# Performance work log

Measured on AMD Instinct MI355X. Metric: run time of the kernel, lower is better.

Reference implementation:

```python
import jax, jax.numpy as jnp
import numpy as np

E, H, NH, FFN, OUT = 4096, 512, 4, 1024, 1
HD = H // NH
LN_EPS = 1e-5


def setup_inputs() -> dict:
    key = jax.random.key(0)
    ks = jax.random.split(key, 20)
    s = 1.0 / np.sqrt(H)
    inp = {
        'x': jax.random.normal(ks[0], (E, H), jnp.float32),
        'edge_index': jax.random.randint(ks[1], (2, E), 0, E, jnp.int64),
        # DMPNN message linear
        'W_msg': jax.random.normal(ks[2], (H, H), jnp.float32) * s,
        'b_msg': jnp.zeros((H,), jnp.float32),
        # GRUCell weights (torch layout: [3H, H], gates r,z,n)
        'W_ih': jax.random.normal(ks[3], (3 * H, H), jnp.float32) * s,
        'b_ih': jnp.zeros((3 * H,), jnp.float32),
        'W_hh': jax.random.normal(ks[4], (3 * H, H), jnp.float32) * s,
        'b_hh': jnp.zeros((3 * H,), jnp.float32),
        # MultiheadAttention combined in-proj [3H, H] and out-proj [H, H]
        'W_in_proj': jax.random.normal(ks[5], (3 * H, H), jnp.float32) * s,
        'b_in_proj': jnp.zeros((3 * H,), jnp.float32),
        'W_out_proj': jax.random.normal(ks[6], (H, H), jnp.float32) * s,
        'b_out_proj': jnp.zeros((H,), jnp.float32),
        # LayerNorm
        'ln_g': jnp.ones((H,), jnp.float32),
        'ln_b': jnp.zeros((H,), jnp.float32),
        # GlobalAttention output linear
        'W_lin': jax.random.normal(ks[7], (H, H), jnp.float32) * s,
        'b_lin': jnp.zeros((H,), jnp.float32),
        # FFN: Linear(H->FFN), ReLU, Linear(FFN->OUT)
        'W_f1': jax.random.normal(ks[8], (FFN, H), jnp.float32) * s,
        'b_f1': jnp.zeros((FFN,), jnp.float32),
        'W_f2': jax.random.normal(ks[9], (OUT, FFN), jnp.float32) * (1.0 / np.sqrt(FFN)),
        'b_f2': jnp.zeros((OUT,), jnp.float32),
    }
    return inp


def reference(x, edge_index, W_msg, b_msg, W_ih, b_ih, W_hh, b_hh,
              W_in_proj, b_in_proj, W_out_proj, b_out_proj, ln_g, ln_b,
              W_lin, b_lin, W_f1, b_f1, W_f2, b_f2):
    # ---- DMPNNLayer: message + scatter-add aggregation + GRUCell update ----
    msg = jax.nn.relu(x @ W_msg.T + b_msg)                       # [E, H]
    agg = jnp.zeros_like(x).at[edge_index[1]].add(msg)           # scatter-add to dst edges
    gi = agg @ W_ih.T + b_ih                                     # [E, 3H]
    gh = x @ W_hh.T + b_hh                                       # [E, 3H]
    ir, iz, inn = jnp.split(gi, 3, axis=-1)
    hr, hz, hn = jnp.split(gh, 3, axis=-1)
    r = jax.nn.sigmoid(ir + hr)
    z = jax.nn.sigmoid(iz + hz)
    n = jnp.tanh(inn + r * hn)
    h = (1.0 - z) * n + z * x                                    # [E, H] updated edges
    # ---- GlobalAttention: MHA(h,h,h) + residual LN + relu(linear) ----
    qkv = h @ W_in_proj.T + b_in_proj                            # [E, 3H]
    q, k, v = jnp.split(qkv, 3, axis=-1)
    split_heads = lambda t: t.reshape(E, NH, HD).transpose(1, 0, 2)  # [NH, E, HD]
    q, k, v = split_heads(q), split_heads(k), split_heads(v)
    scale = np.float32(1.0 / np.sqrt(HD))
    attn = jax.nn.softmax(jnp.einsum('hqd,hkd->hqk', q, k) * scale, axis=-1)
    o = jnp.einsum('hqk,hkd->hqd', attn, v).transpose(1, 0, 2).reshape(E, H)
    o = o @ W_out_proj.T + b_out_proj
    y = o + h
    mu = jnp.mean(y, axis=-1, keepdims=True)
    var = jnp.mean((y - mu) ** 2, axis=-1, keepdims=True)
    yn = (y - mu) / jnp.sqrt(var + LN_EPS) * ln_g + ln_b
    g = jax.nn.relu(yn @ W_lin.T + b_lin)                        # [E, H]
    # ---- FFN ----
    f = jax.nn.relu(g @ W_f1.T + b_f1)                           # [E, FFN]
    return f @ W_f2.T + b_f2                                     # [E, OUT]
```

## Files before the change

### kernel.cpp

```cpp
#include <hip/hip_runtime.h>

typedef unsigned short ushort_t;
typedef __attribute__((ext_vector_type(8))) short short8;
typedef __attribute__((ext_vector_type(4))) float float4v;

#define E_N   4096
#define H_N   512
#define NH_N  4
#define HD_N  128
#define FFN_N 1024
#define H3_N  1536

__device__ __forceinline__ float bf2f(ushort_t u) {
  union { unsigned u; float f; } v; v.u = ((unsigned)u) << 16; return v.f;
}
__device__ __forceinline__ ushort_t f2bf(float f) {
  union { float f; unsigned u; } v; v.f = f;
  unsigned r = v.u + 0x7fffu + ((v.u >> 16) & 1u);
  return (ushort_t)(r >> 16);
}
__device__ __forceinline__ float fexp2(float x) {
  return __builtin_amdgcn_exp2f(x);
}
__device__ __forceinline__ uint4 cvt8(const float* p) {
  float4 a = *(const float4*)p;
  float4 b = *(const float4*)(p + 4);
  union { ushort_t u[8]; uint4 v; } pk;
  pk.u[0] = f2bf(a.x); pk.u[1] = f2bf(a.y); pk.u[2] = f2bf(a.z); pk.u[3] = f2bf(a.w);
  pk.u[4] = f2bf(b.x); pk.u[5] = f2bf(b.y); pk.u[6] = f2bf(b.z); pk.u[7] = f2bf(b.w);
  return pk.v;
}

__device__ __forceinline__ void gload16(const void* g, void* l) {
  __builtin_amdgcn_global_load_lds(
      (const __attribute__((address_space(1))) unsigned*)g,
      (__attribute__((address_space(3))) unsigned*)l, 16, 0, 0);
}

__global__ __launch_bounds__(256) void prep_kernel(
    const float* __restrict__ x,
    const float* __restrict__ wmsg, const float* __restrict__ wih,
    const float* __restrict__ whh,  const float* __restrict__ win,
    const float* __restrict__ wout, const float* __restrict__ wlin,
    const float* __restrict__ wf1,  ushort_t* __restrict__ dst,
    float4* __restrict__ agg)
{
  int b = blockIdx.x;
  if (b < 2048) {
    agg[(size_t)b * 256 + threadIdx.x] = make_float4(0.f, 0.f, 0.f, 0.f);
    return;
  }
  size_t o = ((size_t)(b - 2048) * 256 + threadIdx.x) * 8;
  const float* s;
  if      (o < 2097152) s = x    + o;
  else if (o < 2359296) s = wmsg + (o - 2097152);
  else if (o < 3145728) s = wih  + (o - 2359296);
  else if (o < 3932160) s = whh  + (o - 3145728);
  else if (o < 4718592) s = win  + (o - 3932160);
  else if (o < 4980736) s = wout + (o - 4718592);
  else if (o < 5242880) s = wlin + (o - 4980736);
  else                  s = wf1  + (o - 5242880);
  *(uint4*)(dst + o) = cvt8(s);
}

__global__ __launch_bounds__(256) void cvt_agg_kernel(
    const float* __restrict__ agg, ushort_t* __restrict__ aggb) {
  size_t o = ((size_t)blockIdx.x * 256 + threadIdx.x) * 8;
  *(uint4*)(aggb + o) = cvt8(agg + o);
}

__global__ __launch_bounds__(256) void f2red_kernel(
    const float* __restrict__ pf, const float* __restrict__ b2,
    float* __restrict__ out) {
  int i = blockIdx.x * 256 + threadIdx.x;
  float s = b2[0];
#pragma unroll
  for (int k = 0; k < 32; k++) s += pf[(size_t)i * 32 + k];
  out[i] = s;
}

__global__ __launch_bounds__(256) void amerge_kernel(
    const float* __restrict__ po0, const float* __restrict__ po1,
    const float* __restrict__ mlg, ushort_t* __restrict__ ob) {
  int t = blockIdx.x * 256 + threadIdx.x;
  int row = t >> 6;
  int c8  = (t & 63) * 8;
  int head = c8 >> 7;
  const float* p0 = mlg + ((size_t)(0 * 4 + head) * E_N + row) * 2;
  const float* p1 = mlg + ((size_t)(1 * 4 + head) * E_N + row) * 2;
  float m0 = p0[0], l0 = p0[1], m1 = p1[0], l1 = p1[1];
  float m  = fmaxf(m0, m1);
  float e0 = fexp2(m0 - m), e1 = fexp2(m1 - m);
  float inv = 1.f / (l0 * e0 + l1 * e1);
  float s0 = e0 * inv, s1 = e1 * inv;
  size_t off = (size_t)row * H_N + c8;
  float4 a0 = *(const float4*)(po0 + off);
  float4 a1 = *(const float4*)(po0 + off + 4);
  float4 b0 = *(const float4*)(po1 + off);
  float4 b1 = *(const float4*)(po1 + off + 4);
  union { ushort_t u[8]; uint4 v; } o;
  o.u[0] = f2bf(a0.x * s0 + b0.x * s1); o.u[1] = f2bf(a0.y * s0 + b0.y * s1);
  o.u[2] = f2bf(a0.z * s0 + b0.z * s1); o.u[3] = f2bf(a0.w * s0 + b0.w * s1);
  o.u[4] = f2bf(a1.x * s0 + b1.x * s1); o.u[5] = f2bf(a1.y * s0 + b1.y * s1);
  o.u[6] = f2bf(a1.z * s0 + b1.z * s1); o.u[7] = f2bf(a1.w * s0 + b1.w * s1);
  *(uint4*)(ob + off) = o.v;
}

enum { MODE_MSG = 0, MODE_GI = 1, MODE_GH = 2, MODE_QKV = 3, MODE_OUT = 4,
       MODE_LIN = 5, MODE_F1 = 6 };

template <int MODE, int BM>
__global__ __launch_bounds__(256, (BM == 64 ? 4 : 3)) void gemm_bt(
    const ushort_t* __restrict__ A, const ushort_t* __restrict__ W,
    const float* __restrict__ bias, int K,
    float* __restrict__ outf, ushort_t* __restrict__ outb,
    const int* __restrict__ edge, float* __restrict__ aggf,
    const ushort_t* __restrict__ hres,
    ushort_t* __restrict__ qb, ushort_t* __restrict__ kb,
    ushort_t* __restrict__ vt, const float* __restrict__ wf2)
{
  constexpr int MI   = BM / 32;
  constexpr int ASZ  = BM * 128;
  constexpr int BSZ  = 64 * 128;
  constexpr int NCHA = BM / 8;
  constexpr int NCH  = NCHA + 8;

  __shared__ ushort_t As[2][BM * 64];
  __shared__ ushort_t Bs[2][64 * 64];

  const int tid  = threadIdx.x;
  const int lane = tid & 63;
  const int wave = tid >> 6;
  const int quad = lane >> 4;
  const int l15  = lane & 15;
  const int m0 = blockIdx.x * BM;
  const int n0 = blockIdx.y * 64;
  const int wm = (wave >> 1) * (BM / 2);
  const int wn = (wave & 1) * 32;
  const int rmask = (l15 & 7) << 4;

  const int crow  = lane >> 3;
  const int selem = ((((lane & 7) * 16)) ^ (crow << 4)) >> 1;

  float4v acc[MI][2];
#pragma unroll
  for (int i = 0; i < MI; i++)
#pragma unroll
    for (int j = 0; j < 2; j++)
#pragma unroll
      for (int r = 0; r < 4; r++) acc[i][j][r] = 0.f;

#define ISSUE(KK, BUF)                                                         \
  do {                                                                         \
    _Pragma("unroll")                                                          \
    for (int j_ = 0; j_ < NCH / 4; j_++) {                                     \
      const int c_ = wave + j_ * 4;                                            \
      if (c_ < NCHA) {                                                         \
        const int row_ = c_ * 8 + crow;                                        \
        gload16(A + (size_t)(m0 + row_) * K + (KK) + selem,                    \
                (char*)As + (BUF) * ASZ + c_ * 1024);                          \
      } else {                                                                 \
        const int row_ = (c_ - NCHA) * 8 + crow;                               \
        gload16(W + (size_t)(n0 + row_) * K + (KK) + selem,                    \
                (char*)Bs + (BUF) * BSZ + (c_ - NCHA) * 1024);                 \
      }                                                                        \
    }                                                                          \
  } while (0)

  ISSUE(0, 0);
  int cur = 0;

  for (int k0 = 0; k0 < K; k0 += 64) {
    __syncthreads();
    if (k0 + 64 < K) ISSUE(k0 + 64, cur ^ 1);

#pragma unroll
    for (int ks = 0; ks < 2; ks++) {
      short8 af[MI], bfr[2];
#pragma unroll
      for (int i = 0; i < MI; i++)
        af[i] = *(const short8*)((char*)As + cur * ASZ +
                 (wm + i * 16 + l15) * 128 + ((ks * 64 + quad * 16) ^ rmask));
#pragma unroll
      for (int j = 0; j < 2; j++)
        bfr[j] = *(const short8*)((char*)Bs + cur * BSZ +
                 (wn + j * 16 + l15) * 128 + ((ks * 64 + quad * 16) ^ rmask));
#pragma unroll
      for (int i = 0; i < MI; i++)
#pragma unroll
        for (int j = 0; j < 2; j++)
          acc[i][j] = __builtin_amdgcn_mfma_f32_16x16x32_bf16(af[i], bfr[j],
                                                              acc[i][j], 0, 0, 0);
    }
    cur ^= 1;
  }
#undef ISSUE

  if constexpr (MODE == MODE_F1) {
    float fsum[MI][4];
#pragma unroll
    for (int i = 0; i < MI; i++)
#pragma unroll
      for (int r = 0; r < 4; r++) fsum[i][r] = 0.f;
#pragma unroll
    for (int j = 0; j < 2; j++) {
      const int col = n0 + wn + j * 16 + l15;
      const float bv = bias[col];
      const float wv = wf2[col];
#pragma unroll
      for (int i = 0; i < MI; i++)
#pragma unroll
        for (int r = 0; r < 4; r++)
          fsum[i][r] += fmaxf(acc[i][j][r] + bv, 0.f) * wv;
    }
#pragma unroll
    for (int i = 0; i < MI; i++)
#pragma unroll
      for (int r = 0; r < 4; r++) {
        float s = fsum[i][r];
        s += __shfl_xor(s, 1, 64); s += __shfl_xor(s, 2, 64);
        s += __shfl_xor(s, 4, 64); s += __shfl_xor(s, 8, 64);
        if (l15 == 0)
          outf[(size_t)(m0 + wm + i * 16 + quad * 4 + r) * 32 +
               blockIdx.y * 2 + (wave & 1)] = s;
      }
  } else {
#pragma unroll
    for (int j = 0; j < 2; j++) {
      const int col = n0 + wn + j * 16 + l15;
      const float bv = bias[col];
#pragma unroll
      for (int i = 0; i < MI; i++) {
#pragma unroll
        for (int r = 0; r < 4; r++) {
          const int row = m0 + wm + i * 16 + quad * 4 + r;
          float v = acc[i][j][r] + bv;
          if constexpr (MODE == MODE_MSG) {
            v = fmaxf(v, 0.f);
            const int dst = edge[E_N + row] & (E_N - 1);
            atomicAdd(&aggf[(size_t)dst * H_N + col], v);
          } else if constexpr (MODE == MODE_GI || MODE == MODE_GH) {
            outb[(size_t)row * H3_N + col] = f2bf(v);
          } else if constexpr (MODE == MODE_QKV) {
            const int part = col >> 9;
            const int hh   = (col >> 7) & 3;
            const int d    = col & 127;
            if (part == 0) v *= 0.12751749803605814f;
            const ushort_t bvv = f2bf(v);
            if (part == 0)      qb[((size_t)hh * E_N + row) * HD_N + d] = bvv;
            else if (part == 1) kb[((size_t)hh * E_N + row) * HD_N + d] = bvv;
            else                vt[((size_t)hh * HD_N + d) * E_N + row] = bvv;
          } else if constexpr (MODE == MODE_OUT) {
            v += bf2f(hres[(size_t)row * H_N + col]);
            outf[(size_t)row * H_N + col] = v;
          } else {
            outb[(size_t)row * H_N + col] = f2bf(fmaxf(v, 0.f));
          }
        }
      }
    }
  }
}

__global__ __launch_bounds__(256, 2) void attn_kernel(
    const ushort_t* __restrict__ Qg, const ushort_t* __restrict__ Kg,
    const ushort_t* __restrict__ Vtg,
    float* __restrict__ po0, float* __restrict__ po1,
    float* __restrict__ mlg)
{
  const int bid  = blockIdx.x;
  const int head = bid & 3;
  const int half = (bid >> 2) & 1;
  const int qb0  = (bid >> 3) * 64;
  const int tid  = threadIdx.x;
  const int wave = tid >> 6;
  const int lane = tid & 63;
  const int quad = lane >> 4;
  const int l15  = lane & 15;

  __shared__ ushort_t Ks[2][64][128];
  __shared__ ushort_t Vs[2][128][64];
  __shared__ ushort_t Ps[4][16][64];
  char* Psc = (char*)Ps + wave * 2048;

  const ushort_t* Qhead  = Qg  + (size_t)head * E_N * HD_N;
  const ushort_t* Khead  = Kg  + (size_t)head * E_N * HD_N;
  const ushort_t* Vthead = Vtg + (size_t)head * HD_N * E_N;

  short8 aq[4];
#pragma unroll
  for (int ks = 0; ks < 4; ks++)
    aq[ks] = *(const short8*)(Qhead +
        (size_t)(qb0 + wave * 16 + l15) * HD_N + ks * 32 + quad * 8);

  float4v oacc[8];
#pragma unroll
  for (int i = 0; i < 8; i++)
#pragma unroll
    for (int r = 0; r < 4; r++) oacc[i][r] = 0.f;
  float mprev[4], lsum[4];
#pragma unroll
  for (int r = 0; r < 4; r++) { mprev[r] = -1e30f; lsum[r] = 0.f; }

  const int q15sw = (l15 & 7) << 4;
  const int kt0 = half * 2048;

#define ISSUE(KT, BUF)                                                         \
  do {                                                                         \
    char* kb_ = (char*)Ks + ((BUF) << 14);                                     \
    char* vb_ = (char*)Vs + ((BUF) << 14);                                     \
    _Pragma("unroll")                                                          \
    for (int i_ = 0; i_ < 4; i_++) {                                           \
      const int c_ = wave * 4 + i_;                                            \
      const int krow_ = 4 * c_ + (lane >> 4);              \
      gload16(Khead + (size_t)((KT) + krow_) * HD_N +                          \
                  (((((lane & 15) * 16)) ^ ((krow_ & 7) << 4)) >> 1),          \
              kb_ + c_ * 1024);                                                \
      const int vrow_ = 8 * c_ + (lane >> 3);             \
      gload16(Vthead + (size_t)vrow_ * E_N + (KT) +                            \
                  (((((lane & 7) * 16)) ^ ((lane >> 3) << 4)) >> 1),           \
              vb_ + c_ * 1024);                                                \
    }                                                                          \
  } while (0)

  ISSUE(kt0, 0);
  int cur = 0;

  for (int it = 0; it < 32; it++) {
    __syncthreads();
    if (it + 1 < 32) ISSUE(kt0 + (it + 1) * 64, cur ^ 1);

    const char* kt_ = (char*)Ks + (cur << 14);
    const char* vt_ = (char*)Vs + (cur << 14);

    float4v sacc[4];
#pragma unroll
    for (int j = 0; j < 4; j++)
#pragma unroll
      for (int r = 0; r < 4; r++) sacc[j][r] = 0.f;
    __builtin_amdgcn_s_setprio(1);
#pragma unroll
    for (int ks = 0; ks < 4; ks++) {
#pragma unroll
      for (int j = 0; j < 4; j++) {
        short8 bk = *(const short8*)(kt_ + (j * 16 + l15) * 256 +
                                     ((ks * 64 + quad * 16) ^ q15sw));
        sacc[j] = __builtin_amdgcn_mfma_f32_16x16x32_bf16(aq[ks], bk, sacc[j], 0, 0, 0);
      }
    }
    __builtin_amdgcn_s_setprio(0);

    float alpha[4], pv[4][4];
#pragma unroll
    for (int r = 0; r < 4; r++) {
      float mx = -1e30f;
#pragma unroll
      for (int j = 0; j < 4; j++) { float s = sacc[j][r]; pv[j][r] = s; mx = fmaxf(mx, s); }
#pragma unroll
      for (int off = 1; off < 16; off <<= 1) mx = fmaxf(mx, __shfl_xor(mx, off, 64));
      float mnew = fmaxf(mprev[r], mx);
      alpha[r] = fexp2(mprev[r] - mnew);
      float ss = 0.f;
#pragma unroll
      for (int j = 0; j < 4; j++) { float p = fexp2(pv[j][r] - mnew); pv[j][r] = p; ss += p; }
#pragma unroll
      for (int off = 1; off < 16; off <<= 1) ss += __shfl_xor(ss, off, 64);
      lsum[r] = lsum[r] * alpha[r] + ss;
      mprev[r] = mnew;
    }
#pragma unroll
    for (int i = 0; i < 8; i++)
#pragma unroll
      for (int r = 0; r < 4; r++) oacc[i][r] *= alpha[r];

#pragma unroll
    for (int j = 0; j < 4; j++)
#pragma unroll
      for (int r = 0; r < 4; r++) {
        const int prow = quad * 4 + r;
        *(ushort_t*)(Psc + prow * 128 +
                     ((2 * (j * 16 + l15)) ^ ((prow & 7) << 4))) = f2bf(pv[j][r]);
      }

    __builtin_amdgcn_s_setprio(1);
#pragma unroll
    for (int ks2 = 0; ks2 < 2; ks2++) {
      short8 ap = *(const short8*)(Psc + l15 * 128 +
                                   ((ks2 * 64 + quad * 16) ^ q15sw));
#pragma unroll
      for (int j = 0; j < 8; j++) {
        short8 bv = *(const short8*)(vt_ + (j * 16 + l15) * 128 +
                                     ((ks2 * 64 + quad * 16) ^ q15sw));
        oacc[j] = __builtin_amdgcn_mfma_f32_16x16x32_bf16(ap, bv, oacc[j], 0, 0, 0);
      }
    }
    __builtin_amdgcn_s_setprio(0);
    cur ^= 1;
  }
#undef ISSUE

  float* pob = half ? po1 : po0;
#pragma unroll
  for (int j = 0; j < 8; j++)
#pragma unroll
    for (int r = 0; r < 4; r++) {
      const int row = qb0 + wave * 16 + quad * 4 + r;
      const int col = head * HD_N + j * 16 + l15;
      pob[(size_t)row * H_N + col] = oacc[j][r];
    }
  if (l15 == 0) {
#pragma unroll
    for (int r = 0; r < 4; r++) {
      const int row = qb0 + wave * 16 + quad * 4 + r;
      float* mlp = mlg + ((size_t)(half * 4 + head) * E_N + row) * 2;
      mlp[0] = mprev[r];
      mlp[1] = lsum[r];
    }
  }
}

__global__ __launch_bounds__(256) void gru_kernel(
    const ushort_t* __restrict__ gib, const ushort_t* __restrict__ ghb,
    const float* __restrict__ x, ushort_t* __restrict__ hb) {
  int t = blockIdx.x * 256 + threadIdx.x;
  int e = t >> 6, j8 = (t & 63) * 8;
  size_t b = (size_t)e * H3_N + j8;
  short8 vir = *(const short8*)(gib + b);
  short8 viz = *(const short8*)(gib + b + 512);
  short8 vin = *(const short8*)(gib + b + 1024);
  short8 vhr = *(const short8*)(ghb + b);
  short8 vhz = *(const short8*)(ghb + b + 512);
  short8 vhn = *(const short8*)(ghb + b + 1024);
  size_t xo = (size_t)e * H_N + j8;
  float4 x0 = *(const float4*)(x + xo);
  float4 x1 = *(const float4*)(x + xo + 4);
  float xv[8] = {x0.x, x0.y, x0.z, x0.w, x1.x, x1.y, x1.z, x1.w};
  union { ushort_t u[8]; uint4 v; } o;
#pragma unroll
  for (int i = 0; i < 8; i++) {
    float ir = bf2f((ushort_t)vir[i]), iz = bf2f((ushort_t)viz[i]), inn = bf2f((ushort_t)vin[i]);
    float hr = bf2f((ushort_t)vhr[i]), hz = bf2f((ushort_t)vhz[i]), hn  = bf2f((ushort_t)vhn[i]);
    float r = 1.f / (1.f + __expf(-(ir + hr)));
    float z = 1.f / (1.f + __expf(-(iz + hz)));
    float n = tanhf(inn + r * hn);
    o.u[i] = f2bf((1.f - z) * n + z * xv[i]);
  }
  *(uint4*)(hb + xo) = o.v;
}

__global__ __launch_bounds__(256) void ln_kernel(
    const float* __restrict__ y, const float* __restrict__ g,
    const float* __restrict__ b, ushort_t* __restrict__ yn) {
  int wave = threadIdx.x >> 6, lane = threadIdx.x & 63;
  int row = blockIdx.x * 4 + wave;
  const float* yr = y + (size_t)row * H_N;
  float v[8], s = 0.f;
#pragma unroll
  for (int i = 0; i < 8; i++) { v[i] = yr[lane + i * 64]; s += v[i]; }
#pragma unroll
  for (int off = 1; off < 64; off <<= 1) s += __shfl_xor(s, off, 64);
  float mu = s * (1.f / 512.f);
  float q = 0.f;
#pragma unroll
  for (int i = 0; i < 8; i++) { float d = v[i] - mu; q += d * d; }
#pragma unroll
  for (int off = 1; off < 64; off <<= 1) q += __shfl_xor(q, off, 64);
  float rstd = rsqrtf(q * (1.f / 512.f) + 1e-5f);
#pragma unroll
  for (int i = 0; i < 8; i++) {
    int c = lane + i * 64;
    yn[(size_t)row * H_N + c] = f2bf((v[i] - mu) * rstd * g[c] + b[c]);
  }
}

extern "C" void kernel_launch(void* const* d_in, const int* in_sizes, int n_in,
                              void* d_out, int out_size, void* d_ws, size_t ws_size,
                              hipStream_t stream) {
  const float* x     = (const float*)d_in[0];
  const int*   edge  = (const int*)d_in[1];
  const float* W_msg = (const float*)d_in[2];
  const float* b_msg = (const float*)d_in[3];
  const float* W_ih  = (const float*)d_in[4];
  const float* b_ih  = (const float*)d_in[5];
  const float* W_hh  = (const float*)d_in[6];
  const float* b_hh  = (const float*)d_in[7];
  const float* W_in  = (const float*)d_in[8];
  const float* b_in  = (const float*)d_in[9];
  const float* W_out = (const float*)d_in[10];
  const float* b_out = (const float*)d_in[11];
  const float* ln_g  = (const float*)d_in[12];
  const float* ln_b  = (const float*)d_in[13];
  const float* W_lin = (const float*)d_in[14];
  const float* b_lin = (const float*)d_in[15];
  const float* W_f1  = (const float*)d_in[16];
  const float* b_f1  = (const float*)d_in[17];
  const float* W_f2  = (const float*)d_in[18];
  const float* b_f2  = (const float*)d_in[19];

  char* ws = (char*)d_ws;
  const size_t MB = 1024 * 1024;
  float*    agg  = (float*)(ws + 1 * MB);
  ushort_t* hb   = (ushort_t*)(ws + 1 * MB);
  ushort_t* gib  = (ushort_t*)(ws + 9 * MB);
  ushort_t* ghb  = (ushort_t*)(ws + 21 * MB);
  ushort_t* Qb   = (ushort_t*)(ws + 5 * MB);
  ushort_t* Kb   = (ushort_t*)(ws + 9 * MB);
  ushort_t* Vt   = (ushort_t*)(ws + 13 * MB);
  ushort_t* ob   = (ushort_t*)(ws + 17 * MB);
  float*    y    = (float*)(ws + 21 * MB);
  ushort_t* ynb  = (ushort_t*)(ws + 29 * MB);
  ushort_t* gb   = (ushort_t*)(ws + 31 * MB);
  ushort_t* aggb = (ushort_t*)(ws + 29 * MB);
  float*    pf   = (float*)(ws + 21 * MB);
  float*    po0  = (float*)(ws + 21 * MB);
  float*    po1  = (float*)(ws + 33 * MB);
  float*    mlg  = (float*)(ws + 41 * MB);
  ushort_t* xb   = (ushort_t*)(ws + 42 * MB);
  ushort_t* Wmsg_b = xb + 2097152;
  ushort_t* Wih_b  = xb + 2359296;
  ushort_t* Whh_b  = xb + 3145728;
  ushort_t* Win_b  = xb + 3932160;
  ushort_t* Wout_b = xb + 4718592;
  ushort_t* Wlin_b = xb + 4980736;
  ushort_t* Wf1_b  = xb + 5242880;

  prep_kernel<<<4864, 256, 0, stream>>>(
      x, W_msg, W_ih, W_hh, W_in, W_out, W_lin, W_f1, xb, (float4*)agg);

  gemm_bt<MODE_MSG, 64><<<dim3(64, 8), 256, 0, stream>>>(
      xb, Wmsg_b, b_msg, H_N, nullptr, nullptr, edge, agg, nullptr,
      nullptr, nullptr, nullptr, nullptr);

  cvt_agg_kernel<<<1024, 256, 0, stream>>>(agg, aggb);

  gemm_bt<MODE_GI, 128><<<dim3(32, 24), 256, 0, stream>>>(
      aggb, Wih_b, b_ih, H_N, nullptr, gib, nullptr, nullptr, nullptr,
      nullptr, nullptr, nullptr, nullptr);

  gemm_bt<MODE_GH, 128><<<dim3(32, 24), 256, 0, stream>>>(
      xb, Whh_b, b_hh, H_N, nullptr, ghb, nullptr, nullptr, nullptr,
      nullptr, nullptr, nullptr, nullptr);

  gru_kernel<<<1024, 256, 0, stream>>>(gib, ghb, x, hb);

  gemm_bt<MODE_QKV, 128><<<dim3(32, 24), 256, 0, stream>>>(
      hb, Win_b, b_in, H_N, nullptr, nullptr, nullptr, nullptr, nullptr,
      Qb, Kb, Vt, nullptr);

  attn_kernel<<<512, 256, 0, stream>>>(Qb, Kb, Vt, po0, po1, mlg);

  amerge_kernel<<<1024, 256, 0, stream>>>(po0, po1, mlg, ob);

  gemm_bt<MODE_OUT, 64><<<dim3(64, 8), 256, 0, stream>>>(
      ob, Wout_b, b_out, H_N, y, nullptr, nullptr, nullptr, hb,
      nullptr, nullptr, nullptr, nullptr);

  ln_kernel<<<1024, 256, 0, stream>>>(y, ln_g, ln_b, ynb);

  gemm_bt<MODE_LIN, 64><<<dim3(64, 8), 256, 0, stream>>>(
      ynb, Wlin_b, b_lin, H_N, nullptr, gb, nullptr, nullptr, nullptr,
      nullptr, nullptr, nullptr, nullptr);

  gemm_bt<MODE_F1, 64><<<dim3(64, 16), 256, 0, stream>>>(
      gb, Wf1_b, b_f1, H_N, pf, nullptr, nullptr, nullptr, nullptr,
      nullptr, nullptr, nullptr, W_f2);

  f2red_kernel<<<16, 256, 0, stream>>>(pf, b_f2, (float*)d_out);
}
```

Before: 281.8 us.

## Double query rows per wave in attention to reuse K/V tiles

Each attention wave now handles two 16-row query sub-tiles (128 query rows per block instead of 64), so every K and V fragment read from shared memory feeds two MFMAs. The grid is halved to 256 blocks, which also halves global K/V tile loads per query. The cost is roughly double the accumulator registers and only 256 blocks on a 256-CU device, which lowers occupancy and latency hiding, and the launch bound of 2 blocks per CU may force register spills.

```diff
diff --git a/kernel.cpp b/kernel.cpp
--- a/kernel.cpp
+++ b/kernel.cpp
@@ -271,7 +271,7 @@
   const int bid  = blockIdx.x;
   const int head = bid & 3;
   const int half = (bid >> 2) & 1;
-  const int qb0  = (bid >> 3) * 64;
+  const int qb0  = (bid >> 3) * 128;
   const int tid  = threadIdx.x;
   const int wave = tid >> 6;
   const int lane = tid & 63;
@@ -280,27 +280,33 @@
 
   __shared__ ushort_t Ks[2][64][128];
   __shared__ ushort_t Vs[2][128][64];
-  __shared__ ushort_t Ps[4][16][64];
-  char* Psc = (char*)Ps + wave * 2048;
+  __shared__ ushort_t Ps[4][32][64];
+  char* Psc = (char*)Ps + wave * 4096;
 
   const ushort_t* Qhead  = Qg  + (size_t)head * E_N * HD_N;
   const ushort_t* Khead  = Kg  + (size_t)head * E_N * HD_N;
   const ushort_t* Vthead = Vtg + (size_t)head * HD_N * E_N;
 
-  short8 aq[4];
-#pragma unroll
-  for (int ks = 0; ks < 4; ks++)
-    aq[ks] = *(const short8*)(Qhead +
-        (size_t)(qb0 + wave * 16 + l15) * HD_N + ks * 32 + quad * 8);
-
-  float4v oacc[8];
-#pragma unroll
-  for (int i = 0; i < 8; i++)
-#pragma unroll
-    for (int r = 0; r < 4; r++) oacc[i][r] = 0.f;
-  float mprev[4], lsum[4];
-#pragma unroll
-  for (int r = 0; r < 4; r++) { mprev[r] = -1e30f; lsum[r] = 0.f; }
+  short8 aq[2][4];
+#pragma unroll
+  for (int s = 0; s < 2; s++)
+#pragma unroll
+    for (int ks = 0; ks < 4; ks++)
+      aq[s][ks] = *(const short8*)(Qhead +
+          (size_t)(qb0 + wave * 32 + s * 16 + l15) * HD_N + ks * 32 + quad * 8);
+
+  float4v oacc[2][8];
+#pragma unroll
+  for (int s = 0; s < 2; s++)
+#pragma unroll
+    for (int i = 0; i < 8; i++)
+#pragma unroll
+      for (int r = 0; r < 4; r++) oacc[s][i][r] = 0.f;
+  float mprev[2][4], lsum[2][4];
+#pragma unroll
+  for (int s = 0; s < 2; s++)
+#pragma unroll
+    for (int r = 0; r < 4; r++) { mprev[s][r] = -1e30f; lsum[s][r] = 0.f; }
 
   const int q15sw = (l15 & 7) << 4;
   const int kt0 = half * 2048;
@@ -333,11 +339,13 @@
     const char* kt_ = (char*)Ks + (cur << 14);
     const char* vt_ = (char*)Vs + (cur << 14);
 
-    float4v sacc[4];
-#pragma unroll
-    for (int j = 0; j < 4; j++)
-#pragma unroll
-      for (int r = 0; r < 4; r++) sacc[j][r] = 0.f;
+    float4v sacc[2][4];
+#pragma unroll
+    for (int s = 0; s < 2; s++)
+#pragma unroll
+      for (int j = 0; j < 4; j++)
+#pragma unroll
+        for (int r = 0; r < 4; r++) sacc[s][j][r] = 0.f;
     __builtin_amdgcn_s_setprio(1);
 #pragma unroll
     for (int ks = 0; ks < 4; ks++) {
@@ -345,53 +353,60 @@
       for (int j = 0; j < 4; j++) {
         short8 bk = *(const short8*)(kt_ + (j * 16 + l15) * 256 +
                                      ((ks * 64 + quad * 16) ^ q15sw));
-        sacc[j] = __builtin_amdgcn_mfma_f32_16x16x32_bf16(aq[ks], bk, sacc[j], 0, 0, 0);
+        sacc[0][j] = __builtin_amdgcn_mfma_f32_16x16x32_bf16(aq[0][ks], bk, sacc[0][j], 0, 0, 0);
+        sacc[1][j] = __builtin_amdgcn_mfma_f32_16x16x32_bf16(aq[1][ks], bk, sacc[1][j], 0, 0, 0);
       }
     }
     __builtin_amdgcn_s_setprio(0);
 
-    float alpha[4], pv[4][4];
-#pragma unroll
-    for (int r = 0; r < 4; r++) {
-      float mx = -1e30f;
-#pragma unroll
-      for (int j = 0; j < 4; j++) { float s = sacc[j][r]; pv[j][r] = s; mx = fmaxf(mx, s); }
-#pragma unroll
-      for (int off = 1; off < 16; off <<= 1) mx = fmaxf(mx, __shfl_xor(mx, off, 64));
-      float mnew = fmaxf(mprev[r], mx);
-      alpha[r] = fexp2(mprev[r] - mnew);
-      float ss = 0.f;
-#pragma unroll
-      for (int j = 0; j < 4; j++) { float p = fexp2(pv[j][r] - mnew); pv[j][r] = p; ss += p; }
-#pragma unroll
-      for (int off = 1; off < 16; off <<= 1) ss += __shfl_xor(ss, off, 64);
-      lsum[r] = lsum[r] * alpha[r] + ss;
-      mprev[r] = mnew;
-    }
-#pragma unroll
-    for (int i = 0; i < 8; i++)
-#pragma unroll
-      for (int r = 0; r < 4; r++) oacc[i][r] *= alpha[r];
-
-#pragma unroll
-    for (int j = 0; j < 4; j++)
+#pragma unroll
+    for (int s = 0; s < 2; s++) {
+      float alpha[4], pv[4][4];
 #pragma unroll
       for (int r = 0; r < 4; r++) {
-        const int prow = quad * 4 + r;
-        *(ushort_t*)(Psc + prow * 128 +
-                     ((2 * (j * 16 + l15)) ^ ((prow & 7) << 4))) = f2bf(pv[j][r]);
-      }
+        float mx = -1e30f;
+#pragma unroll
+        for (int j = 0; j < 4; j++) { float v = sacc[s][j][r]; pv[j][r] = v; mx = fmaxf(mx, v); }
+#pragma unroll
+        for (int off = 1; off < 16; off <<= 1) mx = fmaxf(mx, __shfl_xor(mx, off, 64));
+        float mnew = fmaxf(mprev[s][r], mx);
+        alpha[r] = fexp2(mprev[s][r] - mnew);
+        float ss = 0.f;
+#pragma unroll
+        for (int j = 0; j < 4; j++) { float p = fexp2(pv[j][r] - mnew); pv[j][r] = p; ss += p; }
+#pragma unroll
+        for (int off = 1; off < 16; off <<= 1) ss += __shfl_xor(ss, off, 64);
+        lsum[s][r] = lsum[s][r] * alpha[r] + ss;
+        mprev[s][r] = mnew;
+      }
+#pragma unroll
+      for (int i = 0; i < 8; i++)
+#pragma unroll
+        for (int r = 0; r < 4; r++) oacc[s][i][r] *= alpha[r];
+
+#pragma unroll
+      for (int j = 0; j < 4; j++)
+#pragma unroll
+        for (int r = 0; r < 4; r++) {
+          const int prow = s * 16 + quad * 4 + r;
+          *(ushort_t*)(Psc + prow * 128 +
+                       ((2 * (j * 16 + l15)) ^ ((prow & 7) << 4))) = f2bf(pv[j][r]);
+        }
+    }
 
     __builtin_amdgcn_s_setprio(1);
 #pragma unroll
     for (int ks2 = 0; ks2 < 2; ks2++) {
-      short8 ap = *(const short8*)(Psc + l15 * 128 +
-                                   ((ks2 * 64 + quad * 16) ^ q15sw));
+      short8 ap0 = *(const short8*)(Psc + (0 * 16 + l15) * 128 +
+                                    ((ks2 * 64 + quad * 16) ^ q15sw));
+      short8 ap1 = *(const short8*)(Psc + (1 * 16 + l15) * 128 +
+                                    ((ks2 * 64 + quad * 16) ^ q15sw));
 #pragma unroll
       for (int j = 0; j < 8; j++) {
         short8 bv = *(const short8*)(vt_ + (j * 16 + l15) * 128 +
                                      ((ks2 * 64 + quad * 16) ^ q15sw));
-        oacc[j] = __builtin_amdgcn_mfma_f32_16x16x32_bf16(ap, bv, oacc[j], 0, 0, 0);
+        oacc[0][j] = __builtin_amdgcn_mfma_f32_16x16x32_bf16(ap0, bv, oacc[0][j], 0, 0, 0);
+        oacc[1][j] = __builtin_amdgcn_mfma_f32_16x16x32_bf16(ap1, bv, oacc[1][j], 0, 0, 0);
       }
     }
     __builtin_amdgcn_s_setprio(0);
@@ -401,20 +416,23 @@
 
   float* pob = half ? po1 : po0;
 #pragma unroll
-  for (int j = 0; j < 8; j++)
-#pragma unroll
-    for (int r = 0; r < 4; r++) {
-      const int row = qb0 + wave * 16 + quad * 4 + r;
-      const int col = head * HD_N + j * 16 + l15;
-      pob[(size_t)row * H_N + col] = oacc[j][r];
-    }
-  if (l15 == 0) {
-#pragma unroll
-    for (int r = 0; r < 4; r++) {
-      const int row = qb0 + wave * 16 + quad * 4 + r;
-      float* mlp = mlg + ((size_t)(half * 4 + head) * E_N + row) * 2;
-      mlp[0] = mprev[r];
-      mlp[1] = lsum[r];
+  for (int s = 0; s < 2; s++) {
+#pragma unroll
+    for (int j = 0; j < 8; j++)
+#pragma unroll
+      for (int r = 0; r < 4; r++) {
+        const int row = qb0 + wave * 32 + s * 16 + quad * 4 + r;
+        const int col = head * HD_N + j * 16 + l15;
+        pob[(size_t)row * H_N + col] = oacc[s][j][r];
+      }
+    if (l15 == 0) {
+#pragma unroll
+      for (int r = 0; r < 4; r++) {
+        const int row = qb0 + wave * 32 + s * 16 + quad * 4 + r;
+        float* mlp = mlg + ((size_t)(half * 4 + head) * E_N + row) * 2;
+        mlp[0] = mprev[s][r];
+        mlp[1] = lsum[s][r];
+      }
     }
   }
 }
@@ -547,7 +565,7 @@
       hb, Win_b, b_in, H_N, nullptr, nullptr, nullptr, nullptr, nullptr,
       Qb, Kb, Vt, nullptr);
 
-  attn_kernel<<<512, 256, 0, stream>>>(Qb, Kb, Vt, po0, po1, mlg);
+  attn_kernel<<<256, 256, 0, stream>>>(Qb, Kb, Vt, po0, po1, mlg);
 
   amerge_kernel<<<1024, 256, 0, stream>>>(po0, po1, mlg, ob);
 
```

Result: slower. 303.6 us (+7.7%).
